# Kernel tuning notes

Measured on AMD Instinct MI355X. Metric: run time of the kernel, lower is better.

The kernel has to match this reference:

```python
import jax, jax.numpy as jnp
import numpy as np

N = 50000      # num nodes
E = 1_200_000  # num edges
NID = 92       # node_input_dim
ED = 1         # edge_input_dim
H = 64         # hidden_dim
L = 5          # num_layers
EMB = 64       # embedding_dim
G = 256        # num graphs in batch
EPS = 1e-5


def _glorot(key, shape):
    fan_in, fan_out = shape[-2], shape[-1]
    lim = float(np.sqrt(6.0 / (fan_in + fan_out)))
    return jax.random.uniform(key, shape, jnp.float32, -lim, lim)


def setup_inputs() -> dict:
    key = jax.random.key(0)
    ks = jax.random.split(key, 16)
    inp = {
        "x": jax.random.normal(ks[0], (N, NID), jnp.float32),
        "edge_attr": jax.random.uniform(ks[1], (E, ED), jnp.float32),
        "edge_index": jax.random.randint(ks[2], (2, E), 0, N, jnp.int32),
        "batch": jnp.sort(jax.random.randint(ks[3], (N,), 0, G, jnp.int32)),
        # node embedding
        "node_W": _glorot(ks[4], (NID, H)),
        "node_b": jnp.zeros((H,), jnp.float32),
        # per-layer message net: Linear(2H+ED,H) -> BN -> SiLU -> Linear(H,H)
        "msg_W1": _glorot(ks[5], (L, 2 * H + ED, H)),
        "msg_b1": jnp.zeros((L, H), jnp.float32),
        "msg_g1": jnp.ones((L, H), jnp.float32),
        "msg_be1": jnp.zeros((L, H), jnp.float32),
        "msg_W2": _glorot(ks[6], (L, H, H)),
        "msg_b2": jnp.zeros((L, H), jnp.float32),
        # per-layer update net: Linear(2H,H) -> BN -> SiLU
        "upd_W": _glorot(ks[7], (L, 2 * H, H)),
        "upd_b": jnp.zeros((L, H), jnp.float32),
        "upd_g": jnp.ones((L, H), jnp.float32),
        "upd_be": jnp.zeros((L, H), jnp.float32),
        # output projection
        "out_W": _glorot(ks[8], (H, EMB)),
        "out_b": jnp.zeros((EMB,), jnp.float32),
    }
    return inp


def _bn(z, g, b):
    # BatchNorm1d, training-mode batch statistics (biased variance), eps=1e-5
    mu = jnp.mean(z, axis=0)
    var = jnp.var(z, axis=0)
    return (z - mu) * jax.lax.rsqrt(var + EPS) * g + b


def reference(x, edge_attr, node_W, node_b, msg_W1, msg_b1, msg_g1, msg_be1,
              msg_W2, msg_b2, upd_W, upd_b, upd_g, upd_be, out_W, out_b,
              edge_index, batch):
    src, dst = edge_index[0], edge_index[1]  # PyG: x_j = x[src], x_i = x[dst]
    h = x @ node_W + node_b                  # [N, H]
    deg = jax.ops.segment_sum(jnp.ones((E,), h.dtype), dst, num_segments=N)
    deg = jnp.maximum(deg, 1.0)[:, None]     # mean aggregation denominator
    for l in range(L):
        # message: cat([x_i, x_j, edge_attr]) -> Linear -> BN -> SiLU -> Linear
        m = jnp.concatenate([h[dst], h[src], edge_attr], axis=1)  # [E, 2H+ED]
        m = _bn(m @ msg_W1[l] + msg_b1[l], msg_g1[l], msg_be1[l])
        m = jax.nn.silu(m) @ msg_W2[l] + msg_b2[l]                # [E, H]
        # aggregate: scatter-mean to destination nodes
        agg = jax.ops.segment_sum(m, dst, num_segments=N) / deg   # [N, H]
        # update: cat([x, agg]) -> Linear -> BN -> SiLU
        u = jnp.concatenate([h, agg], axis=1) @ upd_W[l] + upd_b[l]
        h = jax.nn.silu(_bn(u, upd_g[l], upd_be[l]))              # [N, H]
    # global mean pool over graphs
    cnt = jnp.maximum(jax.ops.segment_sum(jnp.ones((N,), h.dtype), batch, num_segments=G), 1.0)
    g = jax.ops.segment_sum(h, batch, num_segments=G) / cnt[:, None]  # [G, H]
    return jax.nn.silu(g @ out_W + out_b)                              # [G, EMB]
```

## Files before the change

kernel.cpp:

```cpp
#include <hip/hip_runtime.h>
#include <hip/hip_bf16.h>

#define NN 50000
#define EE 1200000
#define GG 256
#define LL 5

__device__ __forceinline__ float silu_f(float x) {
    return x * __builtin_amdgcn_rcpf(1.0f + __expf(-x));
}
__device__ __forceinline__ int rfl(int x) { return __builtin_amdgcn_readfirstlane(x); }

__global__ __launch_bounds__(256) void k_hist(const int* __restrict__ ei, int* __restrict__ fill, int E) {
    int e = blockIdx.x * 256 + threadIdx.x;
    if (e < E) atomicAdd(&fill[ei[E + e]], 1);
}

__global__ __launch_bounds__(1024) void k_scan(const int* __restrict__ cnt, int* __restrict__ rowptr,
                                               float* __restrict__ degf, int* __restrict__ fill, int n) {
    __shared__ int wsum[16];
    __shared__ int carry_s;
    int tid = threadIdx.x, lane = tid & 63, wid = tid >> 6;
    if (tid == 0) carry_s = 0;
    __syncthreads();
    for (int base = 0; base < n; base += 1024) {
        int i = base + tid;
        int v = (i < n) ? cnt[i] : 0;
        int x = v;
        #pragma unroll
        for (int off = 1; off < 64; off <<= 1) {
            int t = __shfl_up(x, off);
            if (lane >= off) x += t;
        }
        if (lane == 63) wsum[wid] = x;
        __syncthreads();
        if (wid == 0 && lane < 16) {
            int w = wsum[lane];
            #pragma unroll
            for (int off = 1; off < 16; off <<= 1) {
                int t = __shfl_up(w, off);
                if (lane >= off) w += t;
            }
            wsum[lane] = w;
        }
        __syncthreads();
        int waveoff = (wid == 0) ? 0 : wsum[wid - 1];
        int inc = x + waveoff;
        int c = carry_s;
        int chunk_total = wsum[15];
        __syncthreads();
        if (i < n) {
            rowptr[i + 1] = c + inc;
            degf[i] = (float)(v > 0 ? v : 1);
            fill[i] = 0;
        }
        if (tid == 0) {
            if (base == 0) rowptr[0] = 0;
            carry_s = c + chunk_total;
        }
        __syncthreads();
    }
}

__global__ __launch_bounds__(256) void k_scatter(const int* __restrict__ ei, const float* __restrict__ ea,
                                                 const int* __restrict__ rowptr, int* __restrict__ fill,
                                                 unsigned int* __restrict__ edata, int E) {
    int e = blockIdx.x * 256 + threadIdx.x;
    if (e < E) {
        int d = ei[E + e];
        int pos = atomicAdd(&fill[d], 1);
        int idx = rowptr[d] + pos;
        int ea15 = (int)(ea[e] * 32768.0f + 0.5f);
        if (ea15 > 32767) ea15 = 32767;
        edata[idx] = ((unsigned int)ea15 << 17) | (unsigned int)ei[e];
    }
}

__global__ __launch_bounds__(256) void k_fold(const float* __restrict__ msg_W2, const float* __restrict__ msg_b2,
                                              const float* __restrict__ upd_W, float* __restrict__ W2p,
                                              float* __restrict__ b2p) {
    int l = blockIdx.x;
    const float* W2 = msg_W2 + (size_t)l * 4096;
    const float* U2 = upd_W + (size_t)l * 8192 + 4096;
    int lane = threadIdx.x & 63, wid = threadIdx.x >> 6;
    for (int ii = 0; ii < 16; ii++) {
        int i = rfl(wid * 16 + ii);
        float acc = 0.0f;
        for (int k = 0; k < 64; k++) acc = fmaf(W2[i * 64 + k], U2[k * 64 + lane], acc);
        W2p[(size_t)l * 4096 + i * 64 + lane] = acc;
    }
    if (wid == 0) {
        float acc = 0.0f;
        for (int k = 0; k < 64; k++) acc = fmaf(msg_b2[l * 64 + k], U2[k * 64 + lane], acc);
        b2p[l * 64 + lane] = acc;
    }
}

__global__ __launch_bounds__(256) void k_node_emb(const float* __restrict__ x, const float* __restrict__ W,
                                                  const float* __restrict__ b, float* __restrict__ h, int n) {
    __shared__ float sW[92 * 64];
    for (int i = threadIdx.x; i < 92 * 64; i += 256) sW[i] = W[i];
    __syncthreads();
    int lane = threadIdx.x & 63;
    int gw = (blockIdx.x * 256 + threadIdx.x) >> 6;
    int nw = (gridDim.x * 256) >> 6;
    float bj = b[lane];
    int tiles = n >> 3;
    for (int t = gw; t < tiles; t += nw) {
        int rb = rfl(t << 3);
        float acc[8];
        #pragma unroll
        for (int r = 0; r < 8; r++) acc[r] = bj;
        for (int kb = 0; kb < 80; kb += 16) {
            float wv[16];
            #pragma unroll
            for (int t2 = 0; t2 < 16; t2++) wv[t2] = sW[(kb + t2) * 64 + lane];
            #pragma unroll
            for (int r = 0; r < 8; r++) {
                const float* xr = x + (size_t)(rb + r) * 92 + kb;
                #pragma unroll
                for (int t2 = 0; t2 < 16; t2++) acc[r] = fmaf(xr[t2], wv[t2], acc[r]);
            }
        }
        {
            float wv[12];
            #pragma unroll
            for (int t2 = 0; t2 < 12; t2++) wv[t2] = sW[(80 + t2) * 64 + lane];
            #pragma unroll
            for (int r = 0; r < 8; r++) {
                const float* xr = x + (size_t)(rb + r) * 92 + 80;
                #pragma unroll
                for (int t2 = 0; t2 < 12; t2++) acc[r] = fmaf(xr[t2], wv[t2], acc[r]);
            }
        }
        #pragma unroll
        for (int r = 0; r < 8; r++) h[(size_t)(rb + r) * 64 + lane] = acc[r];
    }
}

__global__ __launch_bounds__(256) void k_node_pre(const float* __restrict__ h, const float* __restrict__ W1,
                                                  const float* __restrict__ b1, float* __restrict__ Hd,
                                                  _Float16* __restrict__ Hs, int n) {
    __shared__ float sA[4096], sB[4096];
    for (int i = threadIdx.x; i < 4096; i += 256) { sA[i] = W1[i]; sB[i] = W1[4096 + i]; }
    __syncthreads();
    int lane = threadIdx.x & 63;
    int gw = (blockIdx.x * 256 + threadIdx.x) >> 6;
    int nw = (gridDim.x * 256) >> 6;
    float bj = b1[lane];
    int tiles = n >> 3;
    for (int t = gw; t < tiles; t += nw) {
        int rb = rfl(t << 3);
        float accA[8], accB[8];
        #pragma unroll
        for (int r = 0; r < 8; r++) { accA[r] = bj; accB[r] = 0.0f; }
        for (int kb = 0; kb < 64; kb += 16) {
            float wA[16], wB[16];
            #pragma unroll
            for (int t2 = 0; t2 < 16; t2++) { wA[t2] = sA[(kb + t2) * 64 + lane]; wB[t2] = sB[(kb + t2) * 64 + lane]; }
            #pragma unroll
            for (int r = 0; r < 8; r++) {
                const float* hr = h + (size_t)(rb + r) * 64 + kb;
                #pragma unroll
                for (int t2 = 0; t2 < 16; t2++) {
                    float hk = hr[t2];
                    accA[r] = fmaf(hk, wA[t2], accA[r]);
                    accB[r] = fmaf(hk, wB[t2], accB[r]);
                }
            }
        }
        #pragma unroll
        for (int r = 0; r < 8; r++) {
            Hd[(size_t)(rb + r) * 64 + lane] = accA[r];
            Hs[(size_t)(rb + r) * 64 + lane] = (_Float16)accB[r];
        }
    }
}

__global__ __launch_bounds__(256) void k_edge_stats(const float* __restrict__ Hd, const _Float16* __restrict__ Hs,
                                                    const int* __restrict__ rowptr, const unsigned int* __restrict__ edata,
                                                    const float* __restrict__ w1e,
                                                    float* __restrict__ esum, float* __restrict__ esq, int n) {
    __shared__ float rs[4][64], rq[4][64];
    int wid = threadIdx.x >> 6, lane = threadIdx.x & 63;
    int gw = (blockIdx.x * 256 + threadIdx.x) >> 6;
    int nw = (gridDim.x * 256) >> 6;
    float wj = w1e[lane] * (1.0f / 32768.0f);
    float s = 0.0f, q = 0.0f;
    for (int node = gw; node < n; node += nw) {
        int nu = rfl(node);
        int e0 = rowptr[nu], e1 = rowptr[nu + 1];
        if (e0 == e1) continue;
        float hd = Hd[(size_t)nu * 64 + lane];
        int e = e0;
        for (; e + 8 <= e1; e += 8) {
            float hs[8], av[8];
            #pragma unroll
            for (int j = 0; j < 8; j++) {
                unsigned int p = edata[e + j];
                av[j] = (float)(int)(p >> 17);
                hs[j] = (float)Hs[(((size_t)(p & 0x1FFFFu)) << 6) + (unsigned)lane];
            }
            #pragma unroll
            for (int j = 0; j < 8; j++) {
                float z = fmaf(av[j], wj, hd) + hs[j];
                s += z;
                q = fmaf(z, z, q);
            }
        }
        for (; e < e1; e++) {
            unsigned int p = edata[e];
            float a = (float)(int)(p >> 17);
            float z = fmaf(a, wj, hd) + (float)Hs[(((size_t)(p & 0x1FFFFu)) << 6) + (unsigned)lane];
            s += z;
            q = fmaf(z, z, q);
        }
    }
    rs[wid][lane] = s; rq[wid][lane] = q;
    __syncthreads();
    if (wid == 0) {
        float ts = rs[0][lane] + rs[1][lane] + rs[2][lane] + rs[3][lane];
        float tq = rq[0][lane] + rq[1][lane] + rq[2][lane] + rq[3][lane];
        atomicAdd(&esum[lane], ts);
        atomicAdd(&esq[lane], tq);
    }
}

__global__ __launch_bounds__(256) void k_edge_agg(const float* __restrict__ Hd, const _Float16* __restrict__ Hs,
                                                  const int* __restrict__ rowptr, const unsigned int* __restrict__ edata,
                                                  const float* __restrict__ w1e,
                                                  const float* __restrict__ esum, const float* __restrict__ esq,
                                                  const float* __restrict__ g1, const float* __restrict__ be1,
                                                  const float* __restrict__ degf, float* __restrict__ sacc,
                                                  int n, float invE) {
    int lane = threadIdx.x & 63;
    float mean = esum[lane] * invE;
    float var = esq[lane] * invE - mean * mean;
    float inv = rsqrtf(var + 1e-5f);
    float sc = inv * g1[lane];
    float sh = fmaf(-mean, sc, be1[lane]);
    float wj = w1e[lane] * (1.0f / 32768.0f);
    int gw = (blockIdx.x * 256 + threadIdx.x) >> 6;
    int nw = (gridDim.x * 256) >> 6;
    for (int node = gw; node < n; node += nw) {
        int nu = rfl(node);
        int e0 = rowptr[nu], e1 = rowptr[nu + 1];
        float acc = 0.0f;
        float hd = Hd[(size_t)nu * 64 + lane];
        int e = e0;
        for (; e + 8 <= e1; e += 8) {
            float hs[8], av[8];
            #pragma unroll
            for (int j = 0; j < 8; j++) {
                unsigned int p = edata[e + j];
                av[j] = (float)(int)(p >> 17);
                hs[j] = (float)Hs[(((size_t)(p & 0x1FFFFu)) << 6) + (unsigned)lane];
            }
            #pragma unroll
            for (int j = 0; j < 8; j++) {
                float z = fmaf(av[j], wj, hd) + hs[j];
                acc += silu_f(fmaf(z, sc, sh));
            }
        }
        for (; e < e1; e++) {
            unsigned int p = edata[e];
            float a = (float)(int)(p >> 17);
            float z = fmaf(a, wj, hd) + (float)Hs[(((size_t)(p & 0x1FFFFu)) << 6) + (unsigned)lane];
            acc += silu_f(fmaf(z, sc, sh));
        }
        sacc[(size_t)nu * 64 + lane] = acc / degf[nu];
    }
}

__global__ __launch_bounds__(256) void k_node_upd(const float* __restrict__ h, const float* __restrict__ sacc,
                                                  const float* __restrict__ U1, const float* __restrict__ W2p,
                                                  const float* __restrict__ b2p, const float* __restrict__ ub,
                                                  const int* __restrict__ rowptr, float* __restrict__ u,
                                                  float* __restrict__ usum, float* __restrict__ usq, int n) {
    __shared__ float sU[4096], sP[4096];
    __shared__ float rs[4][64], rq[4][64];
    for (int i = threadIdx.x; i < 4096; i += 256) { sU[i] = U1[i]; sP[i] = W2p[i]; }
    __syncthreads();
    int wid = threadIdx.x >> 6, lane = threadIdx.x & 63;
    int gw = (blockIdx.x * 256 + threadIdx.x) >> 6;
    int nw = (gridDim.x * 256) >> 6;
    float b2j = b2p[lane], ubj = ub[lane];
    float s = 0.0f, q = 0.0f;
    int tiles = n >> 3;
    for (int t = gw; t < tiles; t += nw) {
        int rb = rfl(t << 3);
        float acc[8];
        #pragma unroll
        for (int r = 0; r < 8; r++) {
            int c0 = rowptr[rb + r], c1 = rowptr[rb + r + 1];
            acc[r] = ubj + (c1 > c0 ? b2j : 0.0f);
        }
        for (int kb = 0; kb < 64; kb += 16) {
            float wU[16], wP[16];
            #pragma unroll
            for (int t2 = 0; t2 < 16; t2++) { wU[t2] = sU[(kb + t2) * 64 + lane]; wP[t2] = sP[(kb + t2) * 64 + lane]; }
            #pragma unroll
            for (int r = 0; r < 8; r++) {
                const float* hr = h + (size_t)(rb + r) * 64 + kb;
                const float* sr = sacc + (size_t)(rb + r) * 64 + kb;
                #pragma unroll
                for (int t2 = 0; t2 < 16; t2++) {
                    acc[r] = fmaf(hr[t2], wU[t2], acc[r]);
                    acc[r] = fmaf(sr[t2], wP[t2], acc[r]);
                }
            }
        }
        #pragma unroll
        for (int r = 0; r < 8; r++) {
            u[(size_t)(rb + r) * 64 + lane] = acc[r];
            s += acc[r];
            q = fmaf(acc[r], acc[r], q);
        }
    }
    rs[wid][lane] = s; rq[wid][lane] = q;
    __syncthreads();
    if (wid == 0) {
        float ts = rs[0][lane] + rs[1][lane] + rs[2][lane] + rs[3][lane];
        float tq = rq[0][lane] + rq[1][lane] + rq[2][lane] + rq[3][lane];
        atomicAdd(&usum[lane], ts);
        atomicAdd(&usq[lane], tq);
    }
}

__global__ __launch_bounds__(256) void k_node_bn(const float* __restrict__ u, const float* __restrict__ usum,
                                                 const float* __restrict__ usq, const float* __restrict__ g,
                                                 const float* __restrict__ be, float* __restrict__ h,
                                                 int n, float invN) {
    __shared__ float ssc[64], ssh[64];
    if (threadIdx.x < 64) {
        int j = threadIdx.x;
        float mean = usum[j] * invN;
        float var = usq[j] * invN - mean * mean;
        float inv = rsqrtf(var + 1e-5f);
        float sc = inv * g[j];
        ssc[j] = sc;
        ssh[j] = fmaf(-mean, sc, be[j]);
    }
    __syncthreads();
    int total = n * 64;
    for (int i = blockIdx.x * 256 + threadIdx.x; i < total; i += gridDim.x * 256) {
        int j = i & 63;
        float y = fmaf(u[i], ssc[j], ssh[j]);
        h[i] = silu_f(y);
    }
}

__global__ __launch_bounds__(256) void k_bn_pool(const float* __restrict__ u, const float* __restrict__ usum,
                                                 const float* __restrict__ usq, const float* __restrict__ g,
                                                 const float* __restrict__ be, const int* __restrict__ batch,
                                                 float* __restrict__ gsum, float* __restrict__ gcnt,
                                                 int n, float invN) {
    __shared__ float ssc[64], ssh[64];
    if (threadIdx.x < 64) {
        int j = threadIdx.x;
        float mean = usum[j] * invN;
        float var = usq[j] * invN - mean * mean;
        float inv = rsqrtf(var + 1e-5f);
        float sc = inv * g[j];
        ssc[j] = sc;
        ssh[j] = fmaf(-mean, sc, be[j]);
    }
    __syncthreads();
    int lane = threadIdx.x & 63;
    int gw = (blockIdx.x * 256 + threadIdx.x) >> 6;
    int nw = (gridDim.x * 256) >> 6;
    int per = (n + nw - 1) / nw;
    int start = gw * per;
    int end = start + per; if (end > n) end = n;
    if (start >= end) return;
    float sc = ssc[lane], sh = ssh[lane];
    int cur = batch[start];
    float acc = 0.0f, c = 0.0f;
    for (int i = start; i < end; i++) {
        int b = batch[i];
        if (b != cur) {
            atomicAdd(&gsum[(size_t)cur * 64 + lane], acc);
            if (lane == 0) atomicAdd(&gcnt[cur], c);
            cur = b; acc = 0.0f; c = 0.0f;
        }
        float y = fmaf(u[(size_t)i * 64 + lane], sc, sh);
        acc += silu_f(y);
        c += 1.0f;
    }
    atomicAdd(&gsum[(size_t)cur * 64 + lane], acc);
    if (lane == 0) atomicAdd(&gcnt[cur], c);
}

__global__ __launch_bounds__(256) void k_out(const float* __restrict__ gsum, const float* __restrict__ gcnt,
                                             const float* __restrict__ OW, const float* __restrict__ ob,
                                             float* __restrict__ out, int G) {
    __shared__ float sW[4096];
    for (int i = threadIdx.x; i < 4096; i += 256) sW[i] = OW[i];
    __syncthreads();
    int lane = threadIdx.x & 63;
    int gw = (blockIdx.x * 256 + threadIdx.x) >> 6;
    int nw = (gridDim.x * 256) >> 6;
    for (int g = gw; g < G; g += nw) {
        int gu = rfl(g);
        float c = gcnt[gu]; if (c < 1.0f) c = 1.0f;
        float ci = 1.0f / c;
        float acc = ob[lane];
        const float* gr = gsum + (size_t)gu * 64;
        #pragma unroll
        for (int k = 0; k < 64; k++) acc = fmaf(gr[k] * ci, sW[k * 64 + lane], acc);
        out[(size_t)gu * 64 + lane] = silu_f(acc);
    }
}

extern "C" void kernel_launch(void* const* d_in, const int* in_sizes, int n_in,
                              void* d_out, int out_size, void* d_ws, size_t ws_size,
                              hipStream_t stream) {
    const int N = NN, E = EE, G = GG, L = LL;
    const float* x         = (const float*)d_in[0];
    const float* edge_attr = (const float*)d_in[1];
    const int*   edge_index= (const int*)d_in[2];
    const int*   batch     = (const int*)d_in[3];
    const float* node_W    = (const float*)d_in[4];
    const float* node_b    = (const float*)d_in[5];
    const float* msg_W1    = (const float*)d_in[6];
    const float* msg_b1    = (const float*)d_in[7];
    const float* msg_g1    = (const float*)d_in[8];
    const float* msg_be1   = (const float*)d_in[9];
    const float* msg_W2    = (const float*)d_in[10];
    const float* msg_b2    = (const float*)d_in[11];
    const float* upd_W     = (const float*)d_in[12];
    const float* upd_b     = (const float*)d_in[13];
    const float* upd_g     = (const float*)d_in[14];
    const float* upd_be    = (const float*)d_in[15];
    const float* out_W     = (const float*)d_in[16];
    const float* out_b     = (const float*)d_in[17];
    float* out = (float*)d_out;

    char* ws = (char*)d_ws;
    size_t off = 0;
    auto alloc = [&](size_t b) { size_t o = off; off = (off + b + 255) & ~(size_t)255; return o; };
    float* h    = (float*)(ws + alloc((size_t)N * 64 * 4));
    float* Hd   = (float*)(ws + alloc((size_t)N * 64 * 4));
    _Float16* Hs = (_Float16*)(ws + alloc((size_t)N * 64 * 2));
    float* sacc = (float*)(ws + alloc((size_t)N * 64 * 4));
    unsigned int* edata = (unsigned int*)(ws + alloc((size_t)E * 4));
    int* rowptr = (int*)  (ws + alloc((size_t)(N + 1) * 4));
    float* degf = (float*)(ws + alloc((size_t)N * 4));
    float* W2p  = (float*)(ws + alloc((size_t)L * 4096 * 4));
    float* b2p  = (float*)(ws + alloc((size_t)L * 64 * 4));
    size_t zero_begin = off;
    int*   fill = (int*)  (ws + alloc((size_t)N * 4));
    float* stats= (float*)(ws + alloc((size_t)L * 4 * 64 * 4));
    float* gsum = (float*)(ws + alloc((size_t)(G * 64 + G) * 4));
    size_t zero_end = off;
    float* gcnt = gsum + (size_t)G * 64;
    float* u = Hd;

    hipMemsetAsync(ws + zero_begin, 0, zero_end - zero_begin, stream);

    k_hist<<<(E + 255) / 256, 256, 0, stream>>>(edge_index, fill, E);
    k_scan<<<1, 1024, 0, stream>>>(fill, rowptr, degf, fill, N);
    k_scatter<<<(E + 255) / 256, 256, 0, stream>>>(edge_index, edge_attr, rowptr, fill, edata, E);

    k_fold<<<L, 256, 0, stream>>>(msg_W2, msg_b2, upd_W, W2p, b2p);
    k_node_emb<<<1024, 256, 0, stream>>>(x, node_W, node_b, h, N);

    for (int l = 0; l < L; l++) {
        const float* W1  = msg_W1 + (size_t)l * 129 * 64;
        const float* w1e = W1 + 128 * 64;
        float* esum = stats + (size_t)l * 256;
        float* esq  = esum + 64;
        float* usum = esum + 128;
        float* usq  = esum + 192;
        k_node_pre<<<1024, 256, 0, stream>>>(h, W1, msg_b1 + l * 64, Hd, Hs, N);
        k_edge_stats<<<2048, 256, 0, stream>>>(Hd, Hs, rowptr, edata, w1e, esum, esq, N);
        k_edge_agg<<<2048, 256, 0, stream>>>(Hd, Hs, rowptr, edata, w1e, esum, esq,
                                             msg_g1 + l * 64, msg_be1 + l * 64, degf, sacc, N, 1.0f / E);
        k_node_upd<<<1024, 256, 0, stream>>>(h, sacc, upd_W + (size_t)l * 8192, W2p + (size_t)l * 4096,
                                             b2p + (size_t)l * 64, upd_b + l * 64, rowptr,
                                             u, usum, usq, N);
        if (l < L - 1) {
            k_node_bn<<<2048, 256, 0, stream>>>(u, usum, usq, upd_g + l * 64, upd_be + l * 64, h, N, 1.0f / N);
        } else {
            k_bn_pool<<<256, 256, 0, stream>>>(u, usum, usq, upd_g + l * 64, upd_be + l * 64,
                                               batch, gsum, gcnt, N, 1.0f / N);
        }
    }

    k_out<<<64, 256, 0, stream>>>(gsum, gcnt, out_W, out_b, out, G);
}
```

Measured before the change: 1.362 ms.

## Materialize per-edge pre-activations in fp16 buffer to skip second gather

The stats pass now writes each edge's first-layer pre-activation z as fp16 into a new E×64 buffer, and a new apply pass streams that buffer to run BN, SiLU and mean aggregation. This replaces the second pass's random gather of Hs rows and recomputation. The cost is about 150MB of sequential write plus read per layer, and a fallback path is kept for when the workspace is too small.

```diff
diff --git a/kernel.cpp b/kernel.cpp
--- a/kernel.cpp
+++ b/kernel.cpp
@@ -174,6 +174,93 @@
             Hd[(size_t)(rb + r) * 64 + lane] = accA[r];
             Hs[(size_t)(rb + r) * 64 + lane] = (_Float16)accB[r];
         }
+    }
+}
+
+__global__ __launch_bounds__(256) void k_edge_stats_z(const float* __restrict__ Hd, const _Float16* __restrict__ Hs,
+                                                      const int* __restrict__ rowptr, const unsigned int* __restrict__ edata,
+                                                      const float* __restrict__ w1e, _Float16* __restrict__ zbuf,
+                                                      float* __restrict__ esum, float* __restrict__ esq, int n) {
+    __shared__ float rs[4][64], rq[4][64];
+    int wid = threadIdx.x >> 6, lane = threadIdx.x & 63;
+    int gw = (blockIdx.x * 256 + threadIdx.x) >> 6;
+    int nw = (gridDim.x * 256) >> 6;
+    float wj = w1e[lane] * (1.0f / 32768.0f);
+    float s = 0.0f, q = 0.0f;
+    for (int node = gw; node < n; node += nw) {
+        int nu = rfl(node);
+        int e0 = rowptr[nu], e1 = rowptr[nu + 1];
+        if (e0 == e1) continue;
+        float hd = Hd[(size_t)nu * 64 + lane];
+        int e = e0;
+        for (; e + 8 <= e1; e += 8) {
+            float hs[8], av[8];
+            #pragma unroll
+            for (int j = 0; j < 8; j++) {
+                unsigned int p = edata[e + j];
+                av[j] = (float)(int)(p >> 17);
+                hs[j] = (float)Hs[(((size_t)(p & 0x1FFFFu)) << 6) + (unsigned)lane];
+            }
+            #pragma unroll
+            for (int j = 0; j < 8; j++) {
+                float z = fmaf(av[j], wj, hd) + hs[j];
+                zbuf[(((size_t)(e + j)) << 6) + (unsigned)lane] = (_Float16)z;
+                s += z;
+                q = fmaf(z, z, q);
+            }
+        }
+        for (; e < e1; e++) {
+            unsigned int p = edata[e];
+            float a = (float)(int)(p >> 17);
+            float z = fmaf(a, wj, hd) + (float)Hs[(((size_t)(p & 0x1FFFFu)) << 6) + (unsigned)lane];
+            zbuf[(((size_t)e) << 6) + (unsigned)lane] = (_Float16)z;
+            s += z;
+            q = fmaf(z, z, q);
+        }
+    }
+    rs[wid][lane] = s; rq[wid][lane] = q;
+    __syncthreads();
+    if (wid == 0) {
+        float ts = rs[0][lane] + rs[1][lane] + rs[2][lane] + rs[3][lane];
+        float tq = rq[0][lane] + rq[1][lane] + rq[2][lane] + rq[3][lane];
+        atomicAdd(&esum[lane], ts);
+        atomicAdd(&esq[lane], tq);
+    }
+}
+
+__global__ __launch_bounds__(256) void k_edge_apply(const _Float16* __restrict__ zbuf,
+                                                    const int* __restrict__ rowptr,
+                                                    const float* __restrict__ esum, const float* __restrict__ esq,
+                                                    const float* __restrict__ g1, const float* __restrict__ be1,
+                                                    const float* __restrict__ degf, float* __restrict__ sacc,
+                                                    int n, float invE) {
+    int lane = threadIdx.x & 63;
+    float mean = esum[lane] * invE;
+    float var = esq[lane] * invE - mean * mean;
+    float inv = rsqrtf(var + 1e-5f);
+    float sc = inv * g1[lane];
+    float sh = fmaf(-mean, sc, be1[lane]);
+    int gw = (blockIdx.x * 256 + threadIdx.x) >> 6;
+    int nw = (gridDim.x * 256) >> 6;
+    for (int node = gw; node < n; node += nw) {
+        int nu = rfl(node);
+        int e0 = rowptr[nu], e1 = rowptr[nu + 1];
+        float acc = 0.0f;
+        int e = e0;
+        for (; e + 8 <= e1; e += 8) {
+            float zv[8];
+            #pragma unroll
+            for (int j = 0; j < 8; j++)
+                zv[j] = (float)zbuf[(((size_t)(e + j)) << 6) + (unsigned)lane];
+            #pragma unroll
+            for (int j = 0; j < 8; j++)
+                acc += silu_f(fmaf(zv[j], sc, sh));
+        }
+        for (; e < e1; e++) {
+            float z = (float)zbuf[(((size_t)e) << 6) + (unsigned)lane];
+            acc += silu_f(fmaf(z, sc, sh));
+        }
+        sacc[(size_t)nu * 64 + lane] = acc / degf[nu];
     }
 }
 
@@ -455,6 +542,8 @@
     size_t zero_end = off;
     float* gcnt = gsum + (size_t)G * 64;
     float* u = Hd;
+    _Float16* zbuf = (_Float16*)(ws + alloc((size_t)E * 64 * 2));
+    const bool use_z = (off <= ws_size);
 
     hipMemsetAsync(ws + zero_begin, 0, zero_end - zero_begin, stream);
 
@@ -473,9 +562,15 @@
         float* usum = esum + 128;
         float* usq  = esum + 192;
         k_node_pre<<<1024, 256, 0, stream>>>(h, W1, msg_b1 + l * 64, Hd, Hs, N);
-        k_edge_stats<<<2048, 256, 0, stream>>>(Hd, Hs, rowptr, edata, w1e, esum, esq, N);
-        k_edge_agg<<<2048, 256, 0, stream>>>(Hd, Hs, rowptr, edata, w1e, esum, esq,
-                                             msg_g1 + l * 64, msg_be1 + l * 64, degf, sacc, N, 1.0f / E);
+        if (use_z) {
+            k_edge_stats_z<<<2048, 256, 0, stream>>>(Hd, Hs, rowptr, edata, w1e, zbuf, esum, esq, N);
+            k_edge_apply<<<2048, 256, 0, stream>>>(zbuf, rowptr, esum, esq,
+                                                   msg_g1 + l * 64, msg_be1 + l * 64, degf, sacc, N, 1.0f / E);
+        } else {
+            k_edge_stats<<<2048, 256, 0, stream>>>(Hd, Hs, rowptr, edata, w1e, esum, esq, N);
+            k_edge_agg<<<2048, 256, 0, stream>>>(Hd, Hs, rowptr, edata, w1e, esum, esq,
+                                                 msg_g1 + l * 64, msg_be1 + l * 64, degf, sacc, N, 1.0f / E);
+        }
         k_node_upd<<<1024, 256, 0, stream>>>(h, sacc, upd_W + (size_t)l * 8192, W2p + (size_t)l * 4096,
                                              b2p + (size_t)l * 64, upd_b + l * 64, rowptr,
                                              u, usum, usq, N);
```

After: 1.439 ms. 1.06x slower.
